# Kernel optimization log

Measured on AMD Instinct MI355X. Metric: run time of the kernel, lower is better.

Reference implementation:

```python
import jax, jax.numpy as jnp
import numpy as np

HEADS = 4
DIM_HEAD = 32


def setup_inputs() -> dict:
    key = jax.random.key(0)
    k1, k2, k3 = jax.random.split(key, 3)
    b, dim, h, w = 16, 256, 64, 64
    hidden = HEADS * DIM_HEAD  # 128
    x = jax.random.normal(k1, (b, dim, h, w), dtype=jnp.float32)
    # 1x1 convs are just channel matmuls; store kernels as 2D matrices.
    W_qkv = jax.random.normal(k2, (3 * hidden, dim), dtype=jnp.float32) * 0.02
    W_out = jax.random.normal(k3, (dim, hidden), dtype=jnp.float32) * 0.02
    b_out = jnp.zeros((dim,), dtype=jnp.float32)
    return {"x": x, "W_qkv": W_qkv, "W_out": W_out, "b_out": b_out}


def reference(x, W_qkv, W_out, b_out):
    b, c, h, w = x.shape
    n = h * w
    # 1x1 conv: (b, 3*hidden, h, w) -> view (b, 3, heads, dim_head, n)
    qkv = jnp.einsum('bchw,oc->bohw', x, W_qkv)
    qkv = qkv.reshape(b, 3, HEADS, DIM_HEAD, n)
    q, k, v = qkv[:, 0], qkv[:, 1], qkv[:, 2]  # each (b, heads, dim_head, n)
    k = jax.nn.softmax(k, axis=-1)
    # context: (b, heads, dim_head, dim_head)
    context = jnp.einsum('bhdn,bhen->bhde', k, v)
    # out: (b, heads, dim_head, n)
    out = jnp.einsum('bhde,bhen->bhdn', context, q)
    out = out.reshape(b, HEADS * DIM_HEAD, h, w)
    # to_out 1x1 conv with bias
    y = jnp.einsum('bchw,oc->bohw', out, W_out) + b_out[None, :, None, None]
    return y
```

## Files before the change

kernel.cpp:

```cpp
#include <hip/hip_runtime.h>

typedef __attribute__((ext_vector_type(8))) short short8;
typedef __attribute__((ext_vector_type(4))) float f32x4;
typedef unsigned short u16;
typedef unsigned int u32;


__device__ __forceinline__ u16 f2bf(float f) {
    u32 x = __float_as_uint(f);
    u32 r = (x + 0x7fffu + ((x >> 16) & 1u)) >> 16;
    return (u16)r;
}
__device__ __forceinline__ float bf2f(u16 h) {
    return __uint_as_float(((u32)h) << 16);
}

typedef __attribute__((address_space(1))) u32 as1_u32;
typedef __attribute__((address_space(3))) u32 as3_u32;
__device__ __forceinline__ void gload16(const void* g, void* l) {
    __builtin_amdgcn_global_load_lds((as1_u32*)g, (as3_u32*)l, 16, 0, 0);
}

__global__ __launch_bounds__(256) void k_transpose(const float* __restrict__ x,
                                                   u16* __restrict__ xT,
                                                   const float* __restrict__ W,
                                                   u16* __restrict__ Wb) {
    __shared__ alignas(16) u16 tile[64 * 72];
    int t = threadIdx.x;
    int n0 = blockIdx.x * 64, c0 = blockIdx.y * 64, b = blockIdx.z;

    int flat = (b * 4 + blockIdx.y) * 64 + blockIdx.x;
    if (flat < 96) {
        int idx = flat * 256 + t;
        float4 v = *reinterpret_cast<const float4*>(W + (size_t)idx * 4);
        u32 w0 = (u32)f2bf(v.x) | ((u32)f2bf(v.y) << 16);
        u32 w1 = (u32)f2bf(v.z) | ((u32)f2bf(v.w) << 16);
        uint2 o = {w0, w1};
        *reinterpret_cast<uint2*>(Wb + (size_t)idx * 4) = o;
    }

    int rr = t >> 4, nq = (t & 15) * 4;
#pragma unroll
    for (int i = 0; i < 4; i++) {
        int cl = i * 16 + rr;
        float4 v = *reinterpret_cast<const float4*>(x + ((size_t)(b * 256 + c0 + cl) * 4096 + n0 + nq));
        u32 w0 = (u32)f2bf(v.x) | ((u32)f2bf(v.y) << 16);
        u32 w1 = (u32)f2bf(v.z) | ((u32)f2bf(v.w) << 16);
        uint2 o = {w0, w1};
        int col = nq ^ (((cl >> 3) & 7) << 3);
        *reinterpret_cast<uint2*>(&tile[cl * 72 + col]) = o;
    }
    __syncthreads();
    int r = t >> 3, c8 = (t & 7) * 8;
#pragma unroll
    for (int i = 0; i < 2; i++) {
        int nl = i * 32 + r;
        alignas(16) u16 vals[8];
#pragma unroll
        for (int j = 0; j < 8; j++) {
            int row = c8 + j;
            vals[j] = tile[row * 72 + (nl ^ (((row >> 3) & 7) << 3))];
        }
        *reinterpret_cast<uint4*>(xT + ((size_t)(b * 4096 + n0 + nl) * 256 + c0 + c8)) =
            *reinterpret_cast<const uint4*>(vals);
    }
}

__global__ __launch_bounds__(512, 4) void k_fused(const u16* __restrict__ xT,
                                                  const u16* __restrict__ Wb,
                                                  float* __restrict__ part,
                                                  float* __restrict__ denp) {
    __shared__ alignas(16) char smem[70656];
    u16* sA = (u16*)smem;
    u16* sB = (u16*)(smem + 32768);
    u16* Pl = (u16*)smem;
    u16* Vl = (u16*)(smem + 34816);
    float* dpart = (float*)(smem + 69632);

    int t = threadIdx.x;
    int nt = blockIdx.x, b = blockIdx.y;
    int n0 = nt * 128;
    int lane = t & 63, wv = t >> 6, l16 = lane & 15, lq = lane >> 4;
    int wr = wv >> 1, wc = wv & 1;
    int trow = t >> 3, tc8 = (t & 7) * 8;

    f32x4 acc[4][4];
#pragma unroll
    for (int i = 0; i < 4; i++)
#pragma unroll
        for (int j = 0; j < 4; j++) acc[i][j] = (f32x4){0.f, 0.f, 0.f, 0.f};

    const u16* Asrc = Wb + 128 * 256;
    const u16* Bsrc = xT + (size_t)(b * 4096 + n0) * 256;

    for (int kc = 0; kc < 4; kc++) {
        __syncthreads();
#pragma unroll
        for (int q = 0; q < 4; q++) {
            int row = q * 64 + trow;
            gload16(Asrc + (size_t)row * 256 + kc * 64 + tc8, &sA[row * 64 + tc8]);
        }
#pragma unroll
        for (int q = 0; q < 2; q++) {
            int row = q * 64 + trow;
            gload16(Bsrc + (size_t)row * 256 + kc * 64 + tc8, &sB[row * 64 + tc8]);
        }
        __syncthreads();
#pragma unroll
        for (int ks = 0; ks < 2; ks++) {
            int col = ks * 32 + lq * 8;
            short8 af[4], bfr[4];
#pragma unroll
            for (int i = 0; i < 4; i++)
                af[i] = *reinterpret_cast<const short8*>(&sA[(wr * 64 + i * 16 + l16) * 64 + col]);
#pragma unroll
            for (int j = 0; j < 4; j++)
                bfr[j] = *reinterpret_cast<const short8*>(&sB[(wc * 64 + j * 16 + l16) * 64 + col]);
#pragma unroll
            for (int i = 0; i < 4; i++)
#pragma unroll
                for (int j = 0; j < 4; j++)
                    acc[i][j] = __builtin_amdgcn_mfma_f32_16x16x32_bf16(af[i], bfr[j], acc[i][j], 0, 0, 0);
        }
    }
    __syncthreads();

    if (wr < 2) {
#pragma unroll
        for (int i = 0; i < 4; i++) {
            int rbase = wr * 64 + i * 16 + lq * 4;
            float srow[4] = {0.f, 0.f, 0.f, 0.f};
#pragma unroll
            for (int j = 0; j < 4; j++) {
                int n = wc * 64 + j * 16 + l16;
#pragma unroll
                for (int rr = 0; rr < 4; rr++) {
                    float e = __expf(acc[i][j][rr]);
                    Pl[(rbase + rr) * 136 + n] = f2bf(e);
                    srow[rr] += e;
                }
            }
#pragma unroll
            for (int rr = 0; rr < 4; rr++) {
                float s = srow[rr];
                s += __shfl_xor(s, 1, 64); s += __shfl_xor(s, 2, 64);
                s += __shfl_xor(s, 4, 64); s += __shfl_xor(s, 8, 64);
                if (l16 == 0) dpart[(rbase + rr) * 2 + wc] = s;
            }
        }
    } else {
#pragma unroll
        for (int i = 0; i < 4; i++) {
            int rbase = (wr - 2) * 64 + i * 16 + lq * 4;
#pragma unroll
            for (int j = 0; j < 4; j++) {
                int n = wc * 64 + j * 16 + l16;
#pragma unroll
                for (int rr = 0; rr < 4; rr++)
                    Vl[(rbase + rr) * 136 + n] = f2bf(acc[i][j][rr]);
            }
        }
    }
    __syncthreads();

    int h = wv >> 1, eh = wv & 1;
    f32x4 a2[2];
    a2[0] = (f32x4){0.f, 0.f, 0.f, 0.f};
    a2[1] = (f32x4){0.f, 0.f, 0.f, 0.f};
#pragma unroll
    for (int kk = 0; kk < 4; kk++) {
        int col = kk * 32 + lq * 8;
        short8 bfr = *reinterpret_cast<const short8*>(&Vl[(h * 32 + eh * 16 + l16) * 136 + col]);
#pragma unroll
        for (int i = 0; i < 2; i++) {
            short8 af = *reinterpret_cast<const short8*>(&Pl[(h * 32 + i * 16 + l16) * 136 + col]);
            a2[i] = __builtin_amdgcn_mfma_f32_16x16x32_bf16(af, bfr, a2[i], 0, 0, 0);
        }
    }
    float* pp = part + ((size_t)(b * 32 + nt) * 4 + h) * 1024;
#pragma unroll
    for (int i = 0; i < 2; i++)
#pragma unroll
        for (int rr = 0; rr < 4; rr++)
            pp[(i * 16 + lq * 4 + rr) * 32 + eh * 16 + l16] = a2[i][rr];

    if (t < 128)
        denp[((size_t)b * 128 + t) * 32 + nt] = dpart[t * 2] + dpart[t * 2 + 1];
}

__global__ __launch_bounds__(256) void k_red(const float* __restrict__ part,
                                             const float* __restrict__ denp,
                                             float* __restrict__ C) {
    __shared__ float invd[32];
    int bh = blockIdx.x, seg = blockIdx.y;
    int b = bh >> 2, h = bh & 3;
    int t = threadIdx.x;
    if (t < 32) {
        const float* dp = denp + ((size_t)b * 128 + h * 32 + t) * 32;
        float s = 0.f;
#pragma unroll
        for (int nt = 0; nt < 32; nt++) s += dp[nt];
        invd[t] = 1.0f / s;
    }
    __syncthreads();
    int de = seg * 256 + t;
    float a = 0.f;
#pragma unroll 8
    for (int nt = 0; nt < 32; nt++)
        a += part[((size_t)(b * 32 + nt) * 4 + h) * 1024 + de];
    C[(size_t)bh * 1024 + de] = a * invd[de >> 5];
}

__global__ __launch_bounds__(256) void k_G(const float* __restrict__ C,
                                           const float* __restrict__ Wout,
                                           const u16* __restrict__ Wb,
                                           u16* __restrict__ Gb) {
    __shared__ float Cs[4096];
    __shared__ float Us[2048];
    int b = blockIdx.x, ot = blockIdx.y, ch = blockIdx.z, t = threadIdx.x;
    int o0 = ot * 16;
#pragma unroll
    for (int q = 0; q < 16; q++) {
        int idx = q * 256 + t;
        Cs[idx] = C[(size_t)b * 4096 + idx];
    }
    __syncthreads();
#pragma unroll
    for (int q = 0; q < 8; q++) {
        int idx = q * 256 + t;
        int ol = idx >> 7, he = idx & 127;
        int h = he >> 5, e = he & 31;
        const float* wrow = Wout + (o0 + ol) * 128 + h * 32;
        const float* crow = &Cs[h * 1024 + e];
        float a = 0.f;
#pragma unroll
        for (int d = 0; d < 32; d++) a += wrow[d] * crow[d * 32];
        Us[idx] = a;
    }
    __syncthreads();
    int ol = t >> 4, c0 = ch * 128 + (t & 15) * 8;
    float acc[8];
#pragma unroll
    for (int cc = 0; cc < 8; cc++) acc[cc] = 0.f;
    const float* Ur = &Us[ol * 128];
#pragma unroll 4
    for (int he = 0; he < 128; he++) {
        float u = Ur[he];
        short8 w8 = *reinterpret_cast<const short8*>(Wb + he * 256 + c0);
#pragma unroll
        for (int e = 0; e < 8; e++)
            acc[e] += u * bf2f((u16)w8[e]);
    }
    alignas(16) u16 ob[8];
#pragma unroll
    for (int cc = 0; cc < 8; cc++) ob[cc] = f2bf(acc[cc]);
    *reinterpret_cast<uint4*>(Gb + (size_t)(b * 256 + o0 + ol) * 256 + c0) =
        *reinterpret_cast<const uint4*>(ob);
}

__global__ __launch_bounds__(512, 4) void k_y(const u16* __restrict__ Gb,
                                              const u16* __restrict__ xT,
                                              const float* __restrict__ bout,
                                              float* __restrict__ y) {
    __shared__ alignas(16) u16 sA[256 * 64];
    __shared__ alignas(16) u16 sB[128 * 64];
    int t = threadIdx.x;
    int nt = blockIdx.x, b = blockIdx.y;
    int n0 = nt * 128;
    int lane = t & 63, wv = t >> 6, l16 = lane & 15, lq = lane >> 4;
    int wr = wv >> 1, wc = wv & 1;
    int trow = t >> 3, tc8 = (t & 7) * 8;

    f32x4 acc[4][4];
#pragma unroll
    for (int i = 0; i < 4; i++)
#pragma unroll
        for (int j = 0; j < 4; j++) acc[i][j] = (f32x4){0.f, 0.f, 0.f, 0.f};

    const u16* Asrc = Gb + (size_t)b * 256 * 256;
    const u16* Bsrc = xT + (size_t)(b * 4096 + n0) * 256;

    for (int kc = 0; kc < 4; kc++) {
        __syncthreads();
#pragma unroll
        for (int q = 0; q < 4; q++) {
            int row = q * 64 + trow;
            gload16(Asrc + (size_t)row * 256 + kc * 64 + tc8, &sA[row * 64 + tc8]);
        }
#pragma unroll
        for (int q = 0; q < 2; q++) {
            int row = q * 64 + trow;
            gload16(Bsrc + (size_t)row * 256 + kc * 64 + tc8, &sB[row * 64 + tc8]);
        }
        __syncthreads();
#pragma unroll
        for (int ks = 0; ks < 2; ks++) {
            int col = ks * 32 + lq * 8;
            short8 af[4], bfr[4];
#pragma unroll
            for (int i = 0; i < 4; i++)
                af[i] = *reinterpret_cast<const short8*>(&sA[(wr * 64 + i * 16 + l16) * 64 + col]);
#pragma unroll
            for (int j = 0; j < 4; j++)
                bfr[j] = *reinterpret_cast<const short8*>(&sB[(wc * 64 + j * 16 + l16) * 64 + col]);
#pragma unroll
            for (int i = 0; i < 4; i++)
#pragma unroll
                for (int j = 0; j < 4; j++)
                    acc[i][j] = __builtin_amdgcn_mfma_f32_16x16x32_bf16(af[i], bfr[j], acc[i][j], 0, 0, 0);
        }
    }
#pragma unroll
    for (int i = 0; i < 4; i++) {
        int obase = wr * 64 + i * 16 + lq * 4;
#pragma unroll
        for (int j = 0; j < 4; j++) {
            int n = n0 + wc * 64 + j * 16 + l16;
#pragma unroll
            for (int rr = 0; rr < 4; rr++) {
                int o = obase + rr;
                y[(size_t)(b * 256 + o) * 4096 + n] = acc[i][j][rr] + bout[o];
            }
        }
    }
}

extern "C" void kernel_launch(void* const* d_in, const int* in_sizes, int n_in,
                              void* d_out, int out_size, void* d_ws, size_t ws_size,
                              hipStream_t stream) {
    const float* x    = (const float*)d_in[0];
    const float* Wqkv = (const float*)d_in[1];
    const float* Wout = (const float*)d_in[2];
    const float* bout = (const float*)d_in[3];
    float* y = (float*)d_out;

    char* ws = (char*)d_ws;
    u16*   xT   = (u16*)(ws);
    float* part = (float*)(ws + 33554432);
    float* denp = (float*)(ws + 41943040);
    float* C    = (float*)(ws + 42205184);
    u16*   Gb   = (u16*)(ws + 42467328);
    u16*   Wb   = (u16*)(ws + 44564480);

    k_transpose<<<dim3(64, 4, 16), 256, 0, stream>>>(x, xT, Wqkv, Wb);
    k_fused    <<<dim3(32, 16), 512, 0, stream>>>(xT, Wb, part, denp);
    k_red      <<<dim3(64, 4), 256, 0, stream>>>(part, denp, C);
    k_G        <<<dim3(16, 16, 2), 256, 0, stream>>>(C, Wout, Wb, Gb);
    k_y        <<<dim3(32, 16), 512, 0, stream>>>(Gb, xT, bout, y);
}
```

Before: 170.4 us.

## Replace partial-sum buffer and reduction kernel with atomic accumulation

New measurement: 177.2 us. 4.0% more time.

```diff
diff --git a/kernel.cpp b/kernel.cpp
--- a/kernel.cpp
+++ b/kernel.cpp
@@ -24,7 +24,8 @@
 __global__ __launch_bounds__(256) void k_transpose(const float* __restrict__ x,
                                                    u16* __restrict__ xT,
                                                    const float* __restrict__ W,
-                                                   u16* __restrict__ Wb) {
+                                                   u16* __restrict__ Wb,
+                                                   float* __restrict__ Cz) {
     __shared__ alignas(16) u16 tile[64 * 72];
     int t = threadIdx.x;
     int n0 = blockIdx.x * 64, c0 = blockIdx.y * 64, b = blockIdx.z;
@@ -37,6 +38,8 @@
         u32 w1 = (u32)f2bf(v.z) | ((u32)f2bf(v.w) << 16);
         uint2 o = {w0, w1};
         *reinterpret_cast<uint2*>(Wb + (size_t)idx * 4) = o;
+    } else if (flat < 360) {
+        Cz[(flat - 96) * 256 + t] = 0.f;
     }
 
     int rr = t >> 4, nq = (t & 15) * 4;
@@ -68,8 +71,8 @@
 
 __global__ __launch_bounds__(512, 4) void k_fused(const u16* __restrict__ xT,
                                                   const u16* __restrict__ Wb,
-                                                  float* __restrict__ part,
-                                                  float* __restrict__ denp) {
+                                                  float* __restrict__ C,
+                                                  float* __restrict__ den) {
     __shared__ alignas(16) char smem[70656];
     u16* sA = (u16*)smem;
     u16* sB = (u16*)(smem + 32768);
@@ -177,52 +180,33 @@
             a2[i] = __builtin_amdgcn_mfma_f32_16x16x32_bf16(af, bfr, a2[i], 0, 0, 0);
         }
     }
-    float* pp = part + ((size_t)(b * 32 + nt) * 4 + h) * 1024;
+    float* Cp = C + (size_t)(b * 4 + h) * 1024;
 #pragma unroll
     for (int i = 0; i < 2; i++)
 #pragma unroll
         for (int rr = 0; rr < 4; rr++)
-            pp[(i * 16 + lq * 4 + rr) * 32 + eh * 16 + l16] = a2[i][rr];
+            unsafeAtomicAdd(&Cp[(i * 16 + lq * 4 + rr) * 32 + eh * 16 + l16], a2[i][rr]);
 
     if (t < 128)
-        denp[((size_t)b * 128 + t) * 32 + nt] = dpart[t * 2] + dpart[t * 2 + 1];
-}
-
-__global__ __launch_bounds__(256) void k_red(const float* __restrict__ part,
-                                             const float* __restrict__ denp,
-                                             float* __restrict__ C) {
-    __shared__ float invd[32];
-    int bh = blockIdx.x, seg = blockIdx.y;
-    int b = bh >> 2, h = bh & 3;
-    int t = threadIdx.x;
-    if (t < 32) {
-        const float* dp = denp + ((size_t)b * 128 + h * 32 + t) * 32;
-        float s = 0.f;
-#pragma unroll
-        for (int nt = 0; nt < 32; nt++) s += dp[nt];
-        invd[t] = 1.0f / s;
-    }
-    __syncthreads();
-    int de = seg * 256 + t;
-    float a = 0.f;
-#pragma unroll 8
-    for (int nt = 0; nt < 32; nt++)
-        a += part[((size_t)(b * 32 + nt) * 4 + h) * 1024 + de];
-    C[(size_t)bh * 1024 + de] = a * invd[de >> 5];
+        unsafeAtomicAdd(&den[b * 128 + t], dpart[t * 2] + dpart[t * 2 + 1]);
 }
 
 __global__ __launch_bounds__(256) void k_G(const float* __restrict__ C,
+                                           const float* __restrict__ den,
                                            const float* __restrict__ Wout,
                                            const u16* __restrict__ Wb,
                                            u16* __restrict__ Gb) {
     __shared__ float Cs[4096];
     __shared__ float Us[2048];
+    __shared__ float invd[128];
     int b = blockIdx.x, ot = blockIdx.y, ch = blockIdx.z, t = threadIdx.x;
     int o0 = ot * 16;
+    if (t < 128) invd[t] = 1.0f / den[b * 128 + t];
+    __syncthreads();
 #pragma unroll
     for (int q = 0; q < 16; q++) {
         int idx = q * 256 + t;
-        Cs[idx] = C[(size_t)b * 4096 + idx];
+        Cs[idx] = C[(size_t)b * 4096 + idx] * invd[idx >> 5];
     }
     __syncthreads();
 #pragma unroll
@@ -336,15 +320,13 @@
 
     char* ws = (char*)d_ws;
     u16*   xT   = (u16*)(ws);
-    float* part = (float*)(ws + 33554432);
-    float* denp = (float*)(ws + 41943040);
-    float* C    = (float*)(ws + 42205184);
-    u16*   Gb   = (u16*)(ws + 42467328);
-    u16*   Wb   = (u16*)(ws + 44564480);
-
-    k_transpose<<<dim3(64, 4, 16), 256, 0, stream>>>(x, xT, Wqkv, Wb);
-    k_fused    <<<dim3(32, 16), 512, 0, stream>>>(xT, Wb, part, denp);
-    k_red      <<<dim3(64, 4), 256, 0, stream>>>(part, denp, C);
-    k_G        <<<dim3(16, 16, 2), 256, 0, stream>>>(C, Wout, Wb, Gb);
+    float* C    = (float*)(ws + 33554432);
+    float* den  = (float*)(ws + 33816576);
+    u16*   Gb   = (u16*)(ws + 33824768);
+    u16*   Wb   = (u16*)(ws + 35921920);
+
+    k_transpose<<<dim3(64, 4, 16), 256, 0, stream>>>(x, xT, Wqkv, Wb, C);
+    k_fused    <<<dim3(32, 16), 512, 0, stream>>>(xT, Wb, C, den);
+    k_G        <<<dim3(16, 16, 2), 256, 0, stream>>>(C, den, Wout, Wb, Gb);
     k_y        <<<dim3(32, 16), 512, 0, stream>>>(Gb, xT, bout, y);
 }
```

## Fuse x transpose/bf16 conversion into QKV kernel and read fp32 weights directly

Applied to the files above, without the earlier changes.

After: 192.7 us. 13.1% more time.

```diff
diff --git a/kernel.cpp b/kernel.cpp
--- a/kernel.cpp
+++ b/kernel.cpp
@@ -15,66 +15,30 @@
     return __uint_as_float(((u32)h) << 16);
 }
 
+__device__ __forceinline__ short8 pack_bf16x8(const float* f) {
+    union { u32 w[4]; short8 s; } u;
+#pragma unroll
+    for (int i = 0; i < 4; i++)
+        asm("v_cvt_pk_bf16_f32 %0, %1, %2" : "=v"(u.w[i]) : "v"(f[2 * i]), "v"(f[2 * i + 1]));
+    return u.s;
+}
+
 typedef __attribute__((address_space(1))) u32 as1_u32;
 typedef __attribute__((address_space(3))) u32 as3_u32;
 __device__ __forceinline__ void gload16(const void* g, void* l) {
     __builtin_amdgcn_global_load_lds((as1_u32*)g, (as3_u32*)l, 16, 0, 0);
 }
 
-__global__ __launch_bounds__(256) void k_transpose(const float* __restrict__ x,
-                                                   u16* __restrict__ xT,
-                                                   const float* __restrict__ W,
-                                                   u16* __restrict__ Wb) {
-    __shared__ alignas(16) u16 tile[64 * 72];
-    int t = threadIdx.x;
-    int n0 = blockIdx.x * 64, c0 = blockIdx.y * 64, b = blockIdx.z;
-
-    int flat = (b * 4 + blockIdx.y) * 64 + blockIdx.x;
-    if (flat < 96) {
-        int idx = flat * 256 + t;
-        float4 v = *reinterpret_cast<const float4*>(W + (size_t)idx * 4);
-        u32 w0 = (u32)f2bf(v.x) | ((u32)f2bf(v.y) << 16);
-        u32 w1 = (u32)f2bf(v.z) | ((u32)f2bf(v.w) << 16);
-        uint2 o = {w0, w1};
-        *reinterpret_cast<uint2*>(Wb + (size_t)idx * 4) = o;
-    }
-
-    int rr = t >> 4, nq = (t & 15) * 4;
-#pragma unroll
-    for (int i = 0; i < 4; i++) {
-        int cl = i * 16 + rr;
-        float4 v = *reinterpret_cast<const float4*>(x + ((size_t)(b * 256 + c0 + cl) * 4096 + n0 + nq));
-        u32 w0 = (u32)f2bf(v.x) | ((u32)f2bf(v.y) << 16);
-        u32 w1 = (u32)f2bf(v.z) | ((u32)f2bf(v.w) << 16);
-        uint2 o = {w0, w1};
-        int col = nq ^ (((cl >> 3) & 7) << 3);
-        *reinterpret_cast<uint2*>(&tile[cl * 72 + col]) = o;
-    }
-    __syncthreads();
-    int r = t >> 3, c8 = (t & 7) * 8;
-#pragma unroll
-    for (int i = 0; i < 2; i++) {
-        int nl = i * 32 + r;
-        alignas(16) u16 vals[8];
-#pragma unroll
-        for (int j = 0; j < 8; j++) {
-            int row = c8 + j;
-            vals[j] = tile[row * 72 + (nl ^ (((row >> 3) & 7) << 3))];
-        }
-        *reinterpret_cast<uint4*>(xT + ((size_t)(b * 4096 + n0 + nl) * 256 + c0 + c8)) =
-            *reinterpret_cast<const uint4*>(vals);
-    }
-}
-
-__global__ __launch_bounds__(512, 4) void k_fused(const u16* __restrict__ xT,
-                                                  const u16* __restrict__ Wb,
+__global__ __launch_bounds__(512, 4) void k_fused(const float* __restrict__ x,
+                                                  const float* __restrict__ W,
+                                                  u16* __restrict__ xT,
                                                   float* __restrict__ part,
                                                   float* __restrict__ denp) {
-    __shared__ alignas(16) char smem[70656];
-    u16* sA = (u16*)smem;
-    u16* sB = (u16*)(smem + 32768);
-    u16* Pl = (u16*)smem;
-    u16* Vl = (u16*)(smem + 34816);
+    __shared__ alignas(16) char smem[74752];
+    u16* sX   = (u16*)smem;
+    u16* tile = (u16*)(smem + 65536);
+    u16* Pl   = (u16*)smem;
+    u16* Vl   = (u16*)(smem + 34816);
     float* dpart = (float*)(smem + 69632);
 
     int t = threadIdx.x;
@@ -82,7 +46,40 @@
     int n0 = nt * 128;
     int lane = t & 63, wv = t >> 6, l16 = lane & 15, lq = lane >> 4;
     int wr = wv >> 1, wc = wv & 1;
-    int trow = t >> 3, tc8 = (t & 7) * 8;
+
+    for (int si = 0; si < 8; si++) {
+        int cq = (si & 3) * 64, nh = (si >> 2) * 64;
+        __syncthreads();
+#pragma unroll
+        for (int i = 0; i < 2; i++) {
+            int idx = i * 512 + t;
+            int cl = idx >> 4, nq = (idx & 15) * 4;
+            float4 v = *reinterpret_cast<const float4*>(
+                x + ((size_t)(b * 256 + cq + cl) * 4096 + n0 + nh + nq));
+            u32 w0 = (u32)f2bf(v.x) | ((u32)f2bf(v.y) << 16);
+            u32 w1 = (u32)f2bf(v.z) | ((u32)f2bf(v.w) << 16);
+            uint2 o = {w0, w1};
+            int col = nq ^ (((cl >> 3) & 7) << 3);
+            *reinterpret_cast<uint2*>(&tile[cl * 72 + col]) = o;
+        }
+        __syncthreads();
+        {
+            int nl = t >> 3, c8 = (t & 7) * 8;
+            alignas(16) u16 vals[8];
+#pragma unroll
+            for (int j = 0; j < 8; j++) {
+                int row = c8 + j;
+                vals[j] = tile[row * 72 + (nl ^ (((row >> 3) & 7) << 3))];
+            }
+            *reinterpret_cast<uint4*>(xT + ((size_t)(b * 4096 + n0 + nh + nl) * 256 + cq + c8)) =
+                *reinterpret_cast<const uint4*>(vals);
+            int nloc = nh + nl;
+            int g = (cq + c8) >> 3;
+            *reinterpret_cast<uint4*>(&sX[(nloc * 32 + (g ^ (nloc & 7))) * 8]) =
+                *reinterpret_cast<const uint4*>(vals);
+        }
+    }
+    __syncthreads();
 
     f32x4 acc[4][4];
 #pragma unroll
@@ -90,32 +87,26 @@
 #pragma unroll
         for (int j = 0; j < 4; j++) acc[i][j] = (f32x4){0.f, 0.f, 0.f, 0.f};
 
-    const u16* Asrc = Wb + 128 * 256;
-    const u16* Bsrc = xT + (size_t)(b * 4096 + n0) * 256;
-
+    const float* Wsrc = W + 128 * 256;
     for (int kc = 0; kc < 4; kc++) {
-        __syncthreads();
-#pragma unroll
-        for (int q = 0; q < 4; q++) {
-            int row = q * 64 + trow;
-            gload16(Asrc + (size_t)row * 256 + kc * 64 + tc8, &sA[row * 64 + tc8]);
-        }
-#pragma unroll
-        for (int q = 0; q < 2; q++) {
-            int row = q * 64 + trow;
-            gload16(Bsrc + (size_t)row * 256 + kc * 64 + tc8, &sB[row * 64 + tc8]);
-        }
-        __syncthreads();
 #pragma unroll
         for (int ks = 0; ks < 2; ks++) {
-            int col = ks * 32 + lq * 8;
+            int col = kc * 64 + ks * 32 + lq * 8;
+            int g = col >> 3;
             short8 af[4], bfr[4];
 #pragma unroll
-            for (int i = 0; i < 4; i++)
-                af[i] = *reinterpret_cast<const short8*>(&sA[(wr * 64 + i * 16 + l16) * 64 + col]);
-#pragma unroll
-            for (int j = 0; j < 4; j++)
-                bfr[j] = *reinterpret_cast<const short8*>(&sB[(wc * 64 + j * 16 + l16) * 64 + col]);
+            for (int i = 0; i < 4; i++) {
+                const float* wp = Wsrc + (size_t)(wr * 64 + i * 16 + l16) * 256 + col;
+                float4 wa = *reinterpret_cast<const float4*>(wp);
+                float4 wb = *reinterpret_cast<const float4*>(wp + 4);
+                float f8[8] = {wa.x, wa.y, wa.z, wa.w, wb.x, wb.y, wb.z, wb.w};
+                af[i] = pack_bf16x8(f8);
+            }
+#pragma unroll
+            for (int j = 0; j < 4; j++) {
+                int n = wc * 64 + j * 16 + l16;
+                bfr[j] = *reinterpret_cast<const short8*>(&sX[(n * 32 + (g ^ (n & 7))) * 8]);
+            }
 #pragma unroll
             for (int i = 0; i < 4; i++)
 #pragma unroll
@@ -213,7 +204,7 @@
 
 __global__ __launch_bounds__(256) void k_G(const float* __restrict__ C,
                                            const float* __restrict__ Wout,
-                                           const u16* __restrict__ Wb,
+                                           const float* __restrict__ Wqkv,
                                            u16* __restrict__ Gb) {
     __shared__ float Cs[4096];
     __shared__ float Us[2048];
@@ -246,10 +237,11 @@
 #pragma unroll 4
     for (int he = 0; he < 128; he++) {
         float u = Ur[he];
-        short8 w8 = *reinterpret_cast<const short8*>(Wb + he * 256 + c0);
-#pragma unroll
-        for (int e = 0; e < 8; e++)
-            acc[e] += u * bf2f((u16)w8[e]);
+        const float* wqp = Wqkv + (size_t)he * 256 + c0;
+        float4 wa = *reinterpret_cast<const float4*>(wqp);
+        float4 wb = *reinterpret_cast<const float4*>(wqp + 4);
+        acc[0] += u * wa.x; acc[1] += u * wa.y; acc[2] += u * wa.z; acc[3] += u * wa.w;
+        acc[4] += u * wb.x; acc[5] += u * wb.y; acc[6] += u * wb.z; acc[7] += u * wb.w;
     }
     alignas(16) u16 ob[8];
 #pragma unroll
@@ -340,11 +332,9 @@
     float* denp = (float*)(ws + 41943040);
     float* C    = (float*)(ws + 42205184);
     u16*   Gb   = (u16*)(ws + 42467328);
-    u16*   Wb   = (u16*)(ws + 44564480);
-
-    k_transpose<<<dim3(64, 4, 16), 256, 0, stream>>>(x, xT, Wqkv, Wb);
-    k_fused    <<<dim3(32, 16), 512, 0, stream>>>(xT, Wb, part, denp);
-    k_red      <<<dim3(64, 4), 256, 0, stream>>>(part, denp, C);
-    k_G        <<<dim3(16, 16, 2), 256, 0, stream>>>(C, Wout, Wb, Gb);
-    k_y        <<<dim3(32, 16), 512, 0, stream>>>(Gb, xT, bout, y);
-}
+
+    k_fused<<<dim3(32, 16), 512, 0, stream>>>(x, Wqkv, xT, part, denp);
+    k_red  <<<dim3(64, 4), 256, 0, stream>>>(part, denp, C);
+    k_G    <<<dim3(16, 16, 2), 256, 0, stream>>>(C, Wout, Wqkv, Gb);
+    k_y    <<<dim3(32, 16), 512, 0, stream>>>(Gb, xT, bout, y);
+}
```
